# Kernel tuning notes

Hardware: AMD Instinct MI355X
Metric: run time of the kernel (lower is better)

The kernel has to match this reference:

```python
import jax, jax.numpy as jnp
import numpy as np

EMBED_DIM = 1024
NUM_HEADS = 16
HEAD_DIM = EMBED_DIM // NUM_HEADS
R_QKV = 256
R_OUT = 256
B, T = 4, 2048


def setup_inputs() -> dict:
    key = jax.random.key(0)
    k1, k2, k3, k4, k5 = jax.random.split(key, 5)
    s = 0.02
    return {
        "x": jax.random.normal(k1, (B, T, EMBED_DIM), dtype=jnp.float32),
        "W_qkv_v": jax.random.normal(k2, (R_QKV, EMBED_DIM), dtype=jnp.float32) * s,
        "W_qkv_u": jax.random.normal(k3, (3 * EMBED_DIM, R_QKV), dtype=jnp.float32) * s,
        "W_o_v": jax.random.normal(k4, (R_OUT, EMBED_DIM), dtype=jnp.float32) * s,
        "W_o_u": jax.random.normal(k5, (EMBED_DIM, R_OUT), dtype=jnp.float32) * s,
    }


def reference(x, W_qkv_v, W_qkv_u, W_o_v, W_o_u):
    Bq, Tq, C = x.shape
    H, D = NUM_HEADS, HEAD_DIM
    # low-rank qkv projection: x @ V^T @ U^T (torch Linear weight is [out,in])
    qkv = (x @ W_qkv_v.T) @ W_qkv_u.T  # [B,T,3C]
    q, k, v = jnp.split(qkv, 3, axis=-1)
    # split heads -> [B,H,T,D]
    q = q.reshape(Bq, Tq, H, D).transpose(0, 2, 1, 3)
    k = k.reshape(Bq, Tq, H, D).transpose(0, 2, 1, 3)
    v = v.reshape(Bq, Tq, H, D).transpose(0, 2, 1, 3)
    scale = 1.0 / jnp.sqrt(jnp.asarray(D, dtype=x.dtype))
    scores = jnp.einsum('bhtd,bhsd->bhts', q, k) * scale  # [B,H,T,T]
    # softmax in fp32 then cast back, matching torch.softmax(dtype=float32)
    attn = jax.nn.softmax(scores.astype(jnp.float32), axis=-1).astype(q.dtype)
    y = jnp.einsum('bhts,bhsd->bhtd', attn, v)  # [B,H,T,D]
    y = y.transpose(0, 2, 1, 3).reshape(Bq, Tq, C)  # merge heads
    # low-rank output projection
    y = (y @ W_o_v.T) @ W_o_u.T
    return y
```

## Files before the change

### kernel.cpp

```cpp
#include <hip/hip_runtime.h>
#include <hip/hip_bf16.h>

typedef __attribute__((ext_vector_type(8))) short short8;
typedef __attribute__((ext_vector_type(4))) float f32x4;
typedef __attribute__((ext_vector_type(8))) float f32x8;
typedef __attribute__((ext_vector_type(16))) float f32x16;
typedef unsigned short u16;
typedef unsigned int u32;

__device__ __forceinline__ void gload_lds16(const void* g, void* l) {
  typedef const __attribute__((address_space(1))) u32 gu32;
  typedef __attribute__((address_space(3))) u32 lu32;
  __builtin_amdgcn_global_load_lds((gu32*)g, (lu32*)l, 16, 0, 0);
}

__device__ __forceinline__ u16 f2bf(float f) {
  union { float f; u32 u; } v; v.f = f;
  u32 u = v.u + 0x7FFFu + ((v.u >> 16) & 1u);
  return (u16)(u >> 16);
}

__device__ __forceinline__ u32 cvtpk(float lo, float hiv) {
  u32 r;
  asm("v_cvt_pk_bf16_f32 %0, %1, %2" : "=v"(r) : "v"(lo), "v"(hiv));
  return r;
}

__device__ __forceinline__ void plswap(u32& a, u32& b) {
  asm("v_permlane32_swap_b32 %0, %1" : "+v"(a), "+v"(b));
}

__device__ __forceinline__ float fexp2(float x) {
#if __has_builtin(__builtin_amdgcn_exp2f)
  return __builtin_amdgcn_exp2f(x);
#else
  return exp2f(x);
#endif
}

__device__ __forceinline__ short8 lds_read8(const u16* base, int byteoff) {
  return *(const short8*)((const char*)base + byteoff);
}

__global__ __launch_bounds__(256) void cast_all_kernel(
    const float* __restrict__ x, const float* __restrict__ wv,
    const float* __restrict__ wu, const float* __restrict__ wov,
    const float* __restrict__ wou, u16* __restrict__ dst) {
  const long N0 = 8388608, N1 = N0 + 262144, N2 = N1 + 786432,
             N3 = N2 + 262144, N4 = N3 + 262144;
  long i = (long)(blockIdx.x * 256 + threadIdx.x) * 8;
  if (i >= N4) return;
  const float* s;
  if (i < N0) s = x + i;
  else if (i < N1) s = wv + (i - N0);
  else if (i < N2) s = wu + (i - N1);
  else if (i < N3) s = wov + (i - N2);
  else s = wou + (i - N3);
  float4 a = *(const float4*)s;
  float4 b = *(const float4*)(s + 4);
  short8 o;
  o[0] = (short)f2bf(a.x); o[1] = (short)f2bf(a.y);
  o[2] = (short)f2bf(a.z); o[3] = (short)f2bf(a.w);
  o[4] = (short)f2bf(b.x); o[5] = (short)f2bf(b.y);
  o[6] = (short)f2bf(b.z); o[7] = (short)f2bf(b.w);
  *(short8*)(dst + i) = o;
}

template<int BM, int BN, int MR, int NR, typename OutT>
__global__ __launch_bounds__(256) void gemm_bt(
    OutT* __restrict__ C, const u16* __restrict__ A, const u16* __restrict__ B,
    int N, int K) {
  __shared__ u16 As[BM * 64];
  __shared__ u16 Bs[BN * 64];
  const int tid = threadIdx.x;
  const int l = tid & 63, w = tid >> 6;
  const int wr = w >> 1, wc = w & 1;
  const int bm = blockIdx.x * BM, bn = blockIdx.y * BN;
  const int srow = l >> 3, sslot = (l & 7) ^ srow;

  f32x4 acc[MR][NR] = {};

  const u16* Ag = A + (long)(bm + srow) * K + sslot * 8;
  const u16* Bg = B + (long)(bn + srow) * K + sslot * 8;
  constexpr int CA = BM / 32, CB = BN / 32;

  for (int kt = 0; kt < K; kt += 64) {
#pragma unroll
    for (int c = 0; c < CA; ++c) {
      int ch = w * CA + c;
      gload_lds16(Ag + (long)ch * 8 * K + kt, (char*)As + ch * 1024);
    }
#pragma unroll
    for (int c = 0; c < CB; ++c) {
      int ch = w * CB + c;
      gload_lds16(Bg + (long)ch * 8 * K + kt, (char*)Bs + ch * 1024);
    }
    __syncthreads();
    short8 af[MR][2], bf[NR][2];
#pragma unroll
    for (int i = 0; i < MR; ++i)
#pragma unroll
      for (int kk = 0; kk < 2; ++kk) {
        int row = wr * (MR * 16) + i * 16 + (l & 15);
        af[i][kk] = lds_read8(As, row * 128 + (((kk * 4 + (l >> 4)) ^ (l & 7)) * 16));
      }
#pragma unroll
    for (int j = 0; j < NR; ++j)
#pragma unroll
      for (int kk = 0; kk < 2; ++kk) {
        int col = wc * (NR * 16) + j * 16 + (l & 15);
        bf[j][kk] = lds_read8(Bs, col * 128 + (((kk * 4 + (l >> 4)) ^ (l & 7)) * 16));
      }
#pragma unroll
    for (int kk = 0; kk < 2; ++kk)
#pragma unroll
      for (int i = 0; i < MR; ++i)
#pragma unroll
        for (int j = 0; j < NR; ++j)
          acc[i][j] = __builtin_amdgcn_mfma_f32_16x16x32_bf16(
              af[i][kk], bf[j][kk], acc[i][j], 0, 0, 0);
    __syncthreads();
  }
#pragma unroll
  for (int i = 0; i < MR; ++i)
#pragma unroll
    for (int j = 0; j < NR; ++j) {
      int row = bm + wr * (MR * 16) + i * 16 + (l >> 4) * 4;
      int col = bn + wc * (NR * 16) + j * 16 + (l & 15);
#pragma unroll
      for (int r = 0; r < 4; ++r) {
        if constexpr (sizeof(OutT) == 4) {
          C[(long)(row + r) * N + col] = acc[i][j][r];
        } else {
          ((u16*)C)[(long)(row + r) * N + col] = f2bf(acc[i][j][r]);
        }
      }
    }
}

__global__ __launch_bounds__(256) void vtrans_kernel(
    u16* __restrict__ Vt, const u16* __restrict__ QKV) {
  constexpr int T = 2048, LDQ = 3072;
  __shared__ u16 L[64 * 80];
  const int tid = threadIdx.x;
  const int t0 = blockIdx.x * 64, bh = blockIdx.y;
  const int b = bh >> 4, h = bh & 15;
  const u16* src = QKV + (long)b * T * LDQ + 2048 + h * 64;
#pragma unroll
  for (int it = 0; it < 2; ++it) {
    int row = (tid >> 3) + it * 32;
    int d0 = (tid & 7) * 8;
    short8 v = *(const short8*)(src + (long)(t0 + row) * LDQ + d0);
#pragma unroll
    for (int j = 0; j < 8; ++j)
      L[(d0 + j) * 80 + row] = (u16)(short)v[j];
  }
  __syncthreads();
  u16* dst = Vt + (long)bh * 64 * T + t0;
#pragma unroll
  for (int it = 0; it < 2; ++it) {
    int d = (tid >> 3) + it * 32;
    int c = (tid & 7) * 8;
    *(short8*)(dst + (long)d * T + c) = *(const short8*)(&L[d * 80 + c]);
  }
}

__global__ __launch_bounds__(256, 4) void attn_kernel(
    u16* __restrict__ Y, const u16* __restrict__ QKV, const u16* __restrict__ Vt) {
  constexpr int T = 2048, LDQ = 3072;
  constexpr float SC = 0.18033688011112042f;
  __shared__ u16 SMEM[16384];
  const int tid = threadIdx.x, l = tid & 63, w = tid >> 6;
  const int lq = l & 31, hi = l >> 5;
  const int qt = blockIdx.x, bh = blockIdx.y;
  const int b = bh >> 4, h = bh & 15;
  const long base = (long)b * T * LDQ;
  const int q0 = qt * 128 + w * 32;

  short8 qf[4];
#pragma unroll
  for (int ks = 0; ks < 4; ++ks)
    qf[ks] = *(const short8*)(QKV + base + (long)(q0 + lq) * LDQ + h * 64 +
                              ks * 16 + hi * 8);

  f32x16 o0 = {}, o1 = {};
  float mrow = -3.0e38f, lrow = 0.0f;

  const int c0 = w * 128, c1 = w * 128 + 64;
  const int kr0 = (c0 + l) >> 3, ds0 = ((c0 + l) & 7) ^ (kr0 & 7);
  const int kr1 = (c1 + l) >> 3, ds1 = ((c1 + l) & 7) ^ (kr1 & 7);
  const u16* Kg = QKV + base + 1024 + h * 64;
  const u16* Vg = Vt + (long)bh * 64 * T;

  auto STAGE = [&](int kt, int s) {
    u16* Kd = SMEM + s * 8192;
    u16* Vd = Kd + 4096;
    gload_lds16(Kg + (long)(kt + kr0) * LDQ + ds0 * 8, (char*)Kd + c0 * 16);
    gload_lds16(Kg + (long)(kt + kr1) * LDQ + ds1 * 8, (char*)Kd + c1 * 16);
    gload_lds16(Vg + (long)kr0 * T + kt + ds0 * 8, (char*)Vd + c0 * 16);
    gload_lds16(Vg + (long)kr1 * T + kt + ds1 * 8, (char*)Vd + c1 * 16);
  };

  const int pslA[4] = {((0 + hi) ^ (lq & 7)) * 16, ((2 + hi) ^ (lq & 7)) * 16,
                       ((4 + hi) ^ (lq & 7)) * 16, ((6 + hi) ^ (lq & 7)) * 16};

  auto COMPUTE = [&](const u16* Ks, const u16* Vs) {
    f32x16 p0 = {}, p1 = {};
#pragma unroll
    for (int ks = 0; ks < 4; ++ks) {
      short8 ka = lds_read8(Ks, lq * 128 + pslA[ks]);
      short8 kb = lds_read8(Ks, (32 + lq) * 128 + pslA[ks]);
      p0 = __builtin_amdgcn_mfma_f32_32x32x16_bf16(ka, qf[ks], p0, 0, 0, 0);
      p1 = __builtin_amdgcn_mfma_f32_32x32x16_bf16(kb, qf[ks], p1, 0, 0, 0);
    }
    f32x16 mv = __builtin_elementwise_max(p0, p1);
    f32x8 m8 = __builtin_elementwise_max(
        __builtin_shufflevector(mv, mv, 0, 1, 2, 3, 4, 5, 6, 7),
        __builtin_shufflevector(mv, mv, 8, 9, 10, 11, 12, 13, 14, 15));
    f32x4 m4 = __builtin_elementwise_max(
        __builtin_shufflevector(m8, m8, 0, 1, 2, 3),
        __builtin_shufflevector(m8, m8, 4, 5, 6, 7));
    float mx = fmaxf(fmaxf(m4[0], m4[1]), fmaxf(m4[2], m4[3]));
    mx = fmaxf(mx, __shfl_xor(mx, 32));
    if (!__all(mx - mrow <= 40.0f)) {
      float mnew = fmaxf(mrow, mx);
      float cr = fexp2((mrow - mnew) * SC);
      mrow = mnew;
      lrow *= cr;
      o0 *= cr;
      o1 *= cr;
    }
    float msc = mrow * SC;
    p0 = p0 * SC - msc;
    p1 = p1 * SC - msc;
#pragma unroll
    for (int r = 0; r < 16; ++r) p0[r] = fexp2(p0[r]);
#pragma unroll
    for (int r = 0; r < 16; ++r) p1[r] = fexp2(p1[r]);
    f32x16 sv = p0 + p1;
    f32x8 s8 = __builtin_shufflevector(sv, sv, 0, 1, 2, 3, 4, 5, 6, 7) +
               __builtin_shufflevector(sv, sv, 8, 9, 10, 11, 12, 13, 14, 15);
    f32x4 s4 = __builtin_shufflevector(s8, s8, 0, 1, 2, 3) +
               __builtin_shufflevector(s8, s8, 4, 5, 6, 7);
    float rs = (s4[0] + s4[1]) + (s4[2] + s4[3]);
    rs += __shfl_xor(rs, 32);
    lrow += rs;
#pragma unroll
    for (int ks = 0; ks < 4; ++ks) {
      const f32x16& ps = (ks < 2) ? p0 : p1;
      const int r0 = (ks & 1) * 8;
      u32 uA = cvtpk(ps[r0 + 0], ps[r0 + 1]);
      u32 uB = cvtpk(ps[r0 + 2], ps[r0 + 3]);
      u32 uC = cvtpk(ps[r0 + 4], ps[r0 + 5]);
      u32 uD = cvtpk(ps[r0 + 6], ps[r0 + 7]);
      plswap(uA, uC);
      plswap(uB, uD);
      union { u32 u[4]; short8 s; } pb;
      pb.u[0] = uA; pb.u[1] = uB; pb.u[2] = uC; pb.u[3] = uD;
      short8 va = lds_read8(Vs, lq * 128 + pslA[ks]);
      short8 vb = lds_read8(Vs, (32 + lq) * 128 + pslA[ks]);
      o0 = __builtin_amdgcn_mfma_f32_32x32x16_bf16(va, pb.s, o0, 0, 0, 0);
      o1 = __builtin_amdgcn_mfma_f32_32x32x16_bf16(vb, pb.s, o1, 0, 0, 0);
    }
  };

  STAGE(0, 0);
  __syncthreads();
  for (int t = 0; t < T / 64; ++t) {
    if (t + 1 < T / 64) STAGE((t + 1) * 64, (t + 1) & 1);
    const u16* Ks = SMEM + (t & 1) * 8192;
    COMPUTE(Ks, Ks + 4096);
    __syncthreads();
  }

  float inv = 1.0f / lrow;
  const int row = w * 32 + lq;
#pragma unroll
  for (int df = 0; df < 2; ++df)
#pragma unroll
    for (int r = 0; r < 16; ++r) {
      int d = df * 32 + (r & 3) + 8 * (r >> 2) + 4 * hi;
      float v = (df ? o1[r] : o0[r]) * inv;
      *(u16*)((char*)SMEM + row * 128 + (((d >> 3) ^ (row & 7)) * 16) + (d & 7) * 2) =
          f2bf(v);
    }
  __syncthreads();
#pragma unroll
  for (int it = 0; it < 4; ++it) {
    int c = tid + it * 256;
    int q = c >> 3, g = c & 7;
    int pg = g ^ (q & 7);
    short8 vv = *(const short8*)((const char*)SMEM + q * 128 + pg * 16);
    *(short8*)(Y + (long)(b * T + qt * 128 + q) * 1024 + h * 64 + g * 8) = vv;
  }
}

__global__ void ws_too_small_kernel(float* out) { out[0] = 3.0e38f; }

extern "C" void kernel_launch(void* const* d_in, const int* in_sizes, int n_in,
                              void* d_out, int out_size, void* d_ws, size_t ws_size,
                              hipStream_t stream) {
  (void)in_sizes; (void)n_in; (void)out_size;
  const float* x   = (const float*)d_in[0];
  const float* wv  = (const float*)d_in[1];
  const float* wu  = (const float*)d_in[2];
  const float* wov = (const float*)d_in[3];
  const float* wou = (const float*)d_in[4];
  float* out = (float*)d_out;
  u16* ws = (u16*)d_ws;

  u16* xb   = ws;
  u16* wvb  = ws + 8388608;
  u16* wub  = ws + 8650752;
  u16* wovb = ws + 9437184;
  u16* woub = ws + 9699328;
  u16* t    = ws + 9961472;
  u16* qkv  = ws + 12058624;
  u16* yb   = ws + 37224448;
  u16* z    = ws + 45613056;
  u16* vt   = xb;

  if (ws_size < 95420416ull) {
    ws_too_small_kernel<<<1, 1, 0, stream>>>(out);
    return;
  }

  cast_all_kernel<<<dim3(4864), dim3(256), 0, stream>>>(x, wv, wu, wov, wou, ws);
  gemm_bt<64, 64, 2, 2, u16><<<dim3(128, 4), dim3(256), 0, stream>>>(t, xb, wvb, 256, 1024);
  gemm_bt<128, 128, 4, 4, u16><<<dim3(64, 24), dim3(256), 0, stream>>>(qkv, t, wub, 3072, 256);
  vtrans_kernel<<<dim3(32, 64), dim3(256), 0, stream>>>(vt, qkv);
  attn_kernel<<<dim3(16, 64), dim3(256), 0, stream>>>(yb, qkv, vt);
  gemm_bt<64, 64, 2, 2, u16><<<dim3(128, 4), dim3(256), 0, stream>>>(z, yb, wovb, 256, 1024);
  gemm_bt<128, 128, 4, 4, float><<<dim3(64, 8), dim3(256), 0, stream>>>(out, z, woub, 1024, 256);
}
```

Before: 180.5 us.

## Fuse x cast into first GEMM, V transpose into QKV GEMM, enlarge attention blocks

Drops the separate fp32-to-bf16 cast of x by converting inside a new first-projection GEMM that loads fp32 A directly. Removes the standalone V-transpose kernel by having the QKV GEMM epilogue write V columns straight into the transposed Vt layout with packed 8-byte stores. The attention kernel moves to 512-thread blocks covering 256 queries, so each K/V tile staged in LDS serves twice as many queries, and it raises wave priority around the MFMA sections. GEMM grids are reordered so the N tile varies fastest. This saves two kernel launches and an extra pass over x and V, at the cost of fewer attention blocks and uncoalesced-ish Vt stores.

Measured after the change: 192.2 us. +6.5%, slower.

```diff
diff --git a/kernel.cpp b/kernel.cpp
--- a/kernel.cpp
+++ b/kernel.cpp
@@ -7,6 +7,7 @@
 typedef __attribute__((ext_vector_type(16))) float f32x16;
 typedef unsigned short u16;
 typedef unsigned int u32;
+typedef unsigned long long u64;
 
 __device__ __forceinline__ void gload_lds16(const void* g, void* l) {
   typedef const __attribute__((address_space(1))) u32 gu32;
@@ -31,31 +32,27 @@
 }
 
 __device__ __forceinline__ float fexp2(float x) {
-#if __has_builtin(__builtin_amdgcn_exp2f)
-  return __builtin_amdgcn_exp2f(x);
-#else
-  return exp2f(x);
-#endif
+  float r;
+  asm("v_exp_f32 %0, %1" : "=v"(r) : "v"(x));
+  return r;
 }
 
 __device__ __forceinline__ short8 lds_read8(const u16* base, int byteoff) {
   return *(const short8*)((const char*)base + byteoff);
 }
 
-__global__ __launch_bounds__(256) void cast_all_kernel(
-    const float* __restrict__ x, const float* __restrict__ wv,
-    const float* __restrict__ wu, const float* __restrict__ wov,
-    const float* __restrict__ wou, u16* __restrict__ dst) {
-  const long N0 = 8388608, N1 = N0 + 262144, N2 = N1 + 786432,
-             N3 = N2 + 262144, N4 = N3 + 262144;
+__global__ __launch_bounds__(256) void cast_w_kernel(
+    const float* __restrict__ wv, const float* __restrict__ wu,
+    const float* __restrict__ wov, const float* __restrict__ wou,
+    u16* __restrict__ dst) {
+  const long N0 = 262144, N1 = N0 + 786432, N2 = N1 + 262144, N3 = N2 + 262144;
   long i = (long)(blockIdx.x * 256 + threadIdx.x) * 8;
-  if (i >= N4) return;
+  if (i >= N3) return;
   const float* s;
-  if (i < N0) s = x + i;
-  else if (i < N1) s = wv + (i - N0);
-  else if (i < N2) s = wu + (i - N1);
-  else if (i < N3) s = wov + (i - N2);
-  else s = wou + (i - N3);
+  if (i < N0) s = wv + i;
+  else if (i < N1) s = wu + (i - N0);
+  else if (i < N2) s = wov + (i - N1);
+  else s = wou + (i - N2);
   float4 a = *(const float4*)s;
   float4 b = *(const float4*)(s + 4);
   short8 o;
@@ -66,16 +63,16 @@
   *(short8*)(dst + i) = o;
 }
 
-template<int BM, int BN, int MR, int NR, typename OutT>
+template<int BM, int BN, int MR, int NR, typename OutT, bool VOUT = false>
 __global__ __launch_bounds__(256) void gemm_bt(
     OutT* __restrict__ C, const u16* __restrict__ A, const u16* __restrict__ B,
-    int N, int K) {
+    int N, int K, u16* __restrict__ Vt = nullptr) {
   __shared__ u16 As[BM * 64];
   __shared__ u16 Bs[BN * 64];
   const int tid = threadIdx.x;
   const int l = tid & 63, w = tid >> 6;
   const int wr = w >> 1, wc = w & 1;
-  const int bm = blockIdx.x * BM, bn = blockIdx.y * BN;
+  const int bm = blockIdx.y * BM, bn = blockIdx.x * BN;
   const int srow = l >> 3, sslot = (l & 7) ^ srow;
 
   f32x4 acc[MR][NR] = {};
@@ -127,45 +124,99 @@
     for (int j = 0; j < NR; ++j) {
       int row = bm + wr * (MR * 16) + i * 16 + (l >> 4) * 4;
       int col = bn + wc * (NR * 16) + j * 16 + (l & 15);
-#pragma unroll
-      for (int r = 0; r < 4; ++r) {
-        if constexpr (sizeof(OutT) == 4) {
-          C[(long)(row + r) * N + col] = acc[i][j][r];
-        } else {
-          ((u16*)C)[(long)(row + r) * N + col] = f2bf(acc[i][j][r]);
+      if (VOUT && col >= 2048) {
+        int hh = (col - 2048) >> 6, d = col & 63;
+        int bq = row >> 11, tq = row & 2047;
+        u64 pk = (u64)f2bf(acc[i][j][0]) | ((u64)f2bf(acc[i][j][1]) << 16) |
+                 ((u64)f2bf(acc[i][j][2]) << 32) | ((u64)f2bf(acc[i][j][3]) << 48);
+        *(u64*)(Vt + ((long)(bq * 16 + hh) * 64 + d) * 2048 + tq) = pk;
+      } else {
+#pragma unroll
+        for (int r = 0; r < 4; ++r) {
+          if constexpr (sizeof(OutT) == 4) {
+            C[(long)(row + r) * N + col] = acc[i][j][r];
+          } else {
+            ((u16*)C)[(long)(row + r) * N + col] = f2bf(acc[i][j][r]);
+          }
         }
       }
     }
 }
 
-__global__ __launch_bounds__(256) void vtrans_kernel(
-    u16* __restrict__ Vt, const u16* __restrict__ QKV) {
-  constexpr int T = 2048, LDQ = 3072;
-  __shared__ u16 L[64 * 80];
+__global__ __launch_bounds__(256) void gemm_a32(
+    u16* __restrict__ C, const float* __restrict__ A, const u16* __restrict__ B,
+    int N, int K) {
+  constexpr int BM = 64, BN = 64, MR = 2, NR = 2;
+  __shared__ u16 As[BM * 64];
+  __shared__ u16 Bs[BN * 64];
   const int tid = threadIdx.x;
-  const int t0 = blockIdx.x * 64, bh = blockIdx.y;
-  const int b = bh >> 4, h = bh & 15;
-  const u16* src = QKV + (long)b * T * LDQ + 2048 + h * 64;
-#pragma unroll
-  for (int it = 0; it < 2; ++it) {
-    int row = (tid >> 3) + it * 32;
-    int d0 = (tid & 7) * 8;
-    short8 v = *(const short8*)(src + (long)(t0 + row) * LDQ + d0);
-#pragma unroll
-    for (int j = 0; j < 8; ++j)
-      L[(d0 + j) * 80 + row] = (u16)(short)v[j];
-  }
-  __syncthreads();
-  u16* dst = Vt + (long)bh * 64 * T + t0;
-#pragma unroll
-  for (int it = 0; it < 2; ++it) {
-    int d = (tid >> 3) + it * 32;
-    int c = (tid & 7) * 8;
-    *(short8*)(dst + (long)d * T + c) = *(const short8*)(&L[d * 80 + c]);
-  }
-}
-
-__global__ __launch_bounds__(256, 4) void attn_kernel(
+  const int l = tid & 63, w = tid >> 6;
+  const int wr = w >> 1, wc = w & 1;
+  const int bm = blockIdx.y * BM, bn = blockIdx.x * BN;
+  const int srow = l >> 3, sslot = (l & 7) ^ srow;
+
+  f32x4 acc[MR][NR] = {};
+  const u16* Bg = B + (long)(bn + srow) * K + sslot * 8;
+
+  for (int kt = 0; kt < K; kt += 64) {
+#pragma unroll
+    for (int c = 0; c < 2; ++c) {
+      int ch = w * 2 + c;
+      gload_lds16(Bg + (long)ch * 8 * K + kt, (char*)Bs + ch * 1024);
+    }
+#pragma unroll
+    for (int it = 0; it < 2; ++it) {
+      int c = tid + it * 256;
+      int row = c >> 3, slot = c & 7;
+      const float* src = A + (long)(bm + row) * K + kt + slot * 8;
+      float4 a = *(const float4*)src;
+      float4 b = *(const float4*)(src + 4);
+      union { u32 u[4]; short8 s; } pk;
+      pk.u[0] = cvtpk(a.x, a.y);
+      pk.u[1] = cvtpk(a.z, a.w);
+      pk.u[2] = cvtpk(b.x, b.y);
+      pk.u[3] = cvtpk(b.z, b.w);
+      *(short8*)((char*)As + row * 128 + ((slot ^ (row & 7)) * 16)) = pk.s;
+    }
+    __syncthreads();
+    short8 af[MR][2], bf[NR][2];
+#pragma unroll
+    for (int i = 0; i < MR; ++i)
+#pragma unroll
+      for (int kk = 0; kk < 2; ++kk) {
+        int row = wr * (MR * 16) + i * 16 + (l & 15);
+        af[i][kk] = lds_read8(As, row * 128 + (((kk * 4 + (l >> 4)) ^ (l & 7)) * 16));
+      }
+#pragma unroll
+    for (int j = 0; j < NR; ++j)
+#pragma unroll
+      for (int kk = 0; kk < 2; ++kk) {
+        int col = wc * (NR * 16) + j * 16 + (l & 15);
+        bf[j][kk] = lds_read8(Bs, col * 128 + (((kk * 4 + (l >> 4)) ^ (l & 7)) * 16));
+      }
+#pragma unroll
+    for (int kk = 0; kk < 2; ++kk)
+#pragma unroll
+      for (int i = 0; i < MR; ++i)
+#pragma unroll
+        for (int j = 0; j < NR; ++j)
+          acc[i][j] = __builtin_amdgcn_mfma_f32_16x16x32_bf16(
+              af[i][kk], bf[j][kk], acc[i][j], 0, 0, 0);
+    __syncthreads();
+  }
+#pragma unroll
+  for (int i = 0; i < MR; ++i)
+#pragma unroll
+    for (int j = 0; j < NR; ++j) {
+      int row = bm + wr * (MR * 16) + i * 16 + (l >> 4) * 4;
+      int col = bn + wc * (NR * 16) + j * 16 + (l & 15);
+#pragma unroll
+      for (int r = 0; r < 4; ++r)
+        C[(long)(row + r) * N + col] = f2bf(acc[i][j][r]);
+    }
+}
+
+__global__ __launch_bounds__(512, 4) void attn_kernel(
     u16* __restrict__ Y, const u16* __restrict__ QKV, const u16* __restrict__ Vt) {
   constexpr int T = 2048, LDQ = 3072;
   constexpr float SC = 0.18033688011112042f;
@@ -175,7 +226,7 @@
   const int qt = blockIdx.x, bh = blockIdx.y;
   const int b = bh >> 4, h = bh & 15;
   const long base = (long)b * T * LDQ;
-  const int q0 = qt * 128 + w * 32;
+  const int q0 = qt * 256 + w * 32;
 
   short8 qf[4];
 #pragma unroll
@@ -186,19 +237,16 @@
   f32x16 o0 = {}, o1 = {};
   float mrow = -3.0e38f, lrow = 0.0f;
 
-  const int c0 = w * 128, c1 = w * 128 + 64;
-  const int kr0 = (c0 + l) >> 3, ds0 = ((c0 + l) & 7) ^ (kr0 & 7);
-  const int kr1 = (c1 + l) >> 3, ds1 = ((c1 + l) & 7) ^ (kr1 & 7);
+  const int c = tid;
+  const int kr = c >> 3, ds = (c & 7) ^ (kr & 7);
   const u16* Kg = QKV + base + 1024 + h * 64;
   const u16* Vg = Vt + (long)bh * 64 * T;
 
   auto STAGE = [&](int kt, int s) {
     u16* Kd = SMEM + s * 8192;
     u16* Vd = Kd + 4096;
-    gload_lds16(Kg + (long)(kt + kr0) * LDQ + ds0 * 8, (char*)Kd + c0 * 16);
-    gload_lds16(Kg + (long)(kt + kr1) * LDQ + ds1 * 8, (char*)Kd + c1 * 16);
-    gload_lds16(Vg + (long)kr0 * T + kt + ds0 * 8, (char*)Vd + c0 * 16);
-    gload_lds16(Vg + (long)kr1 * T + kt + ds1 * 8, (char*)Vd + c1 * 16);
+    gload_lds16(Kg + (long)(kt + kr) * LDQ + ds * 8, (char*)Kd + c * 16);
+    gload_lds16(Vg + (long)kr * T + kt + ds * 8, (char*)Vd + c * 16);
   };
 
   const int pslA[4] = {((0 + hi) ^ (lq & 7)) * 16, ((2 + hi) ^ (lq & 7)) * 16,
@@ -206,6 +254,7 @@
 
   auto COMPUTE = [&](const u16* Ks, const u16* Vs) {
     f32x16 p0 = {}, p1 = {};
+    __builtin_amdgcn_s_setprio(1);
 #pragma unroll
     for (int ks = 0; ks < 4; ++ks) {
       short8 ka = lds_read8(Ks, lq * 128 + pslA[ks]);
@@ -213,6 +262,7 @@
       p0 = __builtin_amdgcn_mfma_f32_32x32x16_bf16(ka, qf[ks], p0, 0, 0, 0);
       p1 = __builtin_amdgcn_mfma_f32_32x32x16_bf16(kb, qf[ks], p1, 0, 0, 0);
     }
+    __builtin_amdgcn_s_setprio(0);
     f32x16 mv = __builtin_elementwise_max(p0, p1);
     f32x8 m8 = __builtin_elementwise_max(
         __builtin_shufflevector(mv, mv, 0, 1, 2, 3, 4, 5, 6, 7),
@@ -245,6 +295,7 @@
     float rs = (s4[0] + s4[1]) + (s4[2] + s4[3]);
     rs += __shfl_xor(rs, 32);
     lrow += rs;
+    __builtin_amdgcn_s_setprio(1);
 #pragma unroll
     for (int ks = 0; ks < 4; ++ks) {
       const f32x16& ps = (ks < 2) ? p0 : p1;
@@ -262,6 +313,7 @@
       o0 = __builtin_amdgcn_mfma_f32_32x32x16_bf16(va, pb.s, o0, 0, 0, 0);
       o1 = __builtin_amdgcn_mfma_f32_32x32x16_bf16(vb, pb.s, o1, 0, 0, 0);
     }
+    __builtin_amdgcn_s_setprio(0);
   };
 
   STAGE(0, 0);
@@ -287,11 +339,11 @@
   __syncthreads();
 #pragma unroll
   for (int it = 0; it < 4; ++it) {
-    int c = tid + it * 256;
-    int q = c >> 3, g = c & 7;
+    int cc = tid + it * 512;
+    int q = cc >> 3, g = cc & 7;
     int pg = g ^ (q & 7);
     short8 vv = *(const short8*)((const char*)SMEM + q * 128 + pg * 16);
-    *(short8*)(Y + (long)(b * T + qt * 128 + q) * 1024 + h * 64 + g * 8) = vv;
+    *(short8*)(Y + (long)(b * T + qt * 256 + q) * 1024 + h * 64 + g * 8) = vv;
   }
 }
 
@@ -309,27 +361,26 @@
   float* out = (float*)d_out;
   u16* ws = (u16*)d_ws;
 
-  u16* xb   = ws;
-  u16* wvb  = ws + 8388608;
-  u16* wub  = ws + 8650752;
-  u16* wovb = ws + 9437184;
-  u16* woub = ws + 9699328;
-  u16* t    = ws + 9961472;
-  u16* qkv  = ws + 12058624;
+  u16* wvb  = ws;
+  u16* wub  = ws + 262144;
+  u16* wovb = ws + 1048576;
+  u16* woub = ws + 1310720;
+  u16* t    = ws + 1572864;
+  u16* qkv  = ws + 3670016;
+  u16* vt   = ws + 28835840;
   u16* yb   = ws + 37224448;
   u16* z    = ws + 45613056;
-  u16* vt   = xb;
 
   if (ws_size < 95420416ull) {
     ws_too_small_kernel<<<1, 1, 0, stream>>>(out);
     return;
   }
 
-  cast_all_kernel<<<dim3(4864), dim3(256), 0, stream>>>(x, wv, wu, wov, wou, ws);
-  gemm_bt<64, 64, 2, 2, u16><<<dim3(128, 4), dim3(256), 0, stream>>>(t, xb, wvb, 256, 1024);
-  gemm_bt<128, 128, 4, 4, u16><<<dim3(64, 24), dim3(256), 0, stream>>>(qkv, t, wub, 3072, 256);
-  vtrans_kernel<<<dim3(32, 64), dim3(256), 0, stream>>>(vt, qkv);
-  attn_kernel<<<dim3(16, 64), dim3(256), 0, stream>>>(yb, qkv, vt);
-  gemm_bt<64, 64, 2, 2, u16><<<dim3(128, 4), dim3(256), 0, stream>>>(z, yb, wovb, 256, 1024);
-  gemm_bt<128, 128, 4, 4, float><<<dim3(64, 8), dim3(256), 0, stream>>>(out, z, woub, 1024, 256);
-}
+  cast_w_kernel<<<dim3(768), dim3(256), 0, stream>>>(wv, wu, wov, wou, ws);
+  gemm_a32<<<dim3(4, 128), dim3(256), 0, stream>>>(t, x, wvb, 256, 1024);
+  gemm_bt<128, 128, 4, 4, u16, true><<<dim3(24, 64), dim3(256), 0, stream>>>(
+      qkv, t, wub, 3072, 256, vt);
+  attn_kernel<<<dim3(8, 64), dim3(512), 0, stream>>>(yb, qkv, vt);
+  gemm_bt<64, 64, 2, 2, u16><<<dim3(4, 128), dim3(256), 0, stream>>>(z, yb, wovb, 256, 1024);
+  gemm_bt<128, 128, 4, 4, float><<<dim3(8, 64), dim3(256), 0, stream>>>(out, z, woub, 1024, 256);
+}
```
